# Optimization experiments

Measured on AMD Instinct MI355X. Metric: run time of the kernel, lower is better.

## Reference

```python
import jax, jax.numpy as jnp
import numpy as np

N, H, E, P = 100000, 64, 1600000, 3


def setup_inputs() -> dict:
    key = jax.random.key(0)
    ks = jax.random.split(key, 12)
    h = jax.random.normal(ks[0], (N, H), dtype=jnp.float32)
    W = jax.random.normal(ks[1], (P, H, H), dtype=jnp.float32) * 0.1
    b = jnp.zeros((P, H), dtype=jnp.float32)
    a = jnp.full((P,), 0.25, dtype=jnp.float32)  # PReLU slopes (torch default init)
    fc_w = jax.random.normal(ks[2], (H, H), dtype=jnp.float32) * 0.1
    fc_b = jnp.zeros((H,), dtype=jnp.float32)
    att = jax.random.normal(ks[3], (H,), dtype=jnp.float32) * 0.1
    adj_vals = jax.random.uniform(ks[4], (E,), dtype=jnp.float32) * (1.0 / 16.0)
    row = jax.random.randint(ks[5], (E,), 0, N, dtype=jnp.int32)
    col = jax.random.randint(ks[6], (E,), 0, N, dtype=jnp.int32)
    mask1 = jax.random.randint(ks[7], (N,), 0, 2, dtype=jnp.int32).astype(bool)
    mask2 = jax.random.randint(ks[8], (N,), 0, 2, dtype=jnp.int32).astype(bool)
    return {"h": h, "W": W, "b": b, "a": a, "fc_w": fc_w, "fc_b": fc_b,
            "att": att, "adj_vals": adj_vals, "row": row, "col": col,
            "mask1": mask1, "mask2": mask2}


def reference(h, W, b, a, fc_w, fc_b, att, adj_vals, row, col, mask1, mask2):
    n = h.shape[0]

    def gcn_all(x):
        # P GCN layers (small fixed P): linear -> spmm(adj) -> +bias -> PReLU
        outs = []
        for p in range(W.shape[0]):
            fts = x @ W[p].T                                   # [N,H]
            msg = fts[col] * adj_vals[:, None]                  # [E,H] gather
            agg = jax.ops.segment_sum(msg, row, num_segments=n) # [N,H] scatter-add
            o = agg + b[p]
            outs.append(jnp.where(o > 0, o, a[p] * o))          # PReLU
        return jnp.stack(outs)                                  # [P,N,H]

    def attention(embeds):
        # sp_p = mean_n tanh(fc(embed_p)); beta = softmax_p(att . sp_p)
        s = jnp.tanh(jnp.einsum('pnh,kh->pnk', embeds, fc_w) + fc_b).mean(axis=1)  # [P,H]
        beta = jax.nn.softmax(s @ att, axis=0)                                      # [P]
        return jnp.einsum('pnh,p->nh', embeds, beta)                                # [N,H]

    h_masked = h * (~mask1)[:, None].astype(h.dtype)
    z_mp = attention(gcn_all(h_masked))       # encode with mask_ratio1
    z_mp2 = attention(gcn_all(h))             # encode with mask_ratio 0
    z_masked = z_mp * (~mask2)[:, None].astype(h.dtype)
    x_recon = attention(gcn_all(z_masked))    # decode
    return (z_mp, z_mp2, x_recon)
```

## Files before the change

kernel.cpp:

```cpp
#include <hip/hip_runtime.h>
#include <hip/hip_bf16.h>

typedef __hip_bfloat16 bf16;
typedef __attribute__((ext_vector_type(8))) short bf16x8;
typedef __attribute__((ext_vector_type(4))) float f32x4;


__device__ __forceinline__ short f2bf(float x) {
    unsigned u = __float_as_uint(x);
    unsigned r = (u + 0x7FFFu + ((u >> 16) & 1u)) >> 16;
    return (short)r;
}
__device__ __forceinline__ float bf2f(short s) {
    return __uint_as_float(((unsigned)(unsigned short)s) << 16);
}
__device__ __forceinline__ void split1(float v, short& h, short& l) {
    h = f2bf(v);
    l = f2bf(v - bf2f(h));
}

__device__ __forceinline__ void split8(const float* __restrict__ p, bool ok, bf16x8& hi,
                                       bf16x8& lo) {
    float v[8];
    if (ok) {
        float4 x0 = ((const float4*)p)[0];
        float4 x1 = ((const float4*)p)[1];
        v[0] = x0.x; v[1] = x0.y; v[2] = x0.z; v[3] = x0.w;
        v[4] = x1.x; v[5] = x1.y; v[6] = x1.z; v[7] = x1.w;
    } else {
#pragma unroll
        for (int j = 0; j < 8; j++) v[j] = 0.f;
    }
#pragma unroll
    for (int j = 0; j < 8; j++) {
        short hb = f2bf(v[j]);
        hi[j] = hb;
        lo[j] = f2bf(v[j] - bf2f(hb));
    }
}

__device__ __forceinline__ float fast_tanh(float x) {
    x = fminf(fmaxf(x, -15.f), 15.f);
    float t = __expf(2.f * x);
    return __fdividef(t - 1.f, t + 1.f);
}

__device__ __forceinline__ void fma4(float4& acc, float v, const float4& x) {
    acc.x = fmaf(v, x.x, acc.x);
    acc.y = fmaf(v, x.y, acc.y);
    acc.z = fmaf(v, x.z, acc.z);
    acc.w = fmaf(v, x.w, acc.w);
}

__device__ __forceinline__ void red4(float4& a) {
    a.x += __shfl_xor(a.x, 16); a.y += __shfl_xor(a.y, 16);
    a.z += __shfl_xor(a.z, 16); a.w += __shfl_xor(a.w, 16);
    a.x += __shfl_xor(a.x, 32); a.y += __shfl_xor(a.y, 32);
    a.z += __shfl_xor(a.z, 32); a.w += __shfl_xor(a.w, 32);
}

__global__ __launch_bounds__(256) void forensic_kernel(const unsigned int* __restrict__ mask_w,
                                                       const unsigned int* __restrict__ idx_w,
                                                       int nw_mask, int nw_idx,
                                                       int* __restrict__ flags) {
    __shared__ int sm[6];
    int t = threadIdx.x;
    if (t < 6) sm[t] = 0;
    __syncthreads();
    int m_gt1 = 0, m_f32 = 0, m_f64 = 0, m_oddnz = 0, i_hi = 0, i_oddnz = 0;
    for (int i = t; i < nw_mask; i += 256) {
        unsigned int w = mask_w[i];
        if (w > 1u && w != 0x3F800000u && w != 0x3FF00000u) m_gt1++;
        if (w == 0x3F800000u) m_f32++;
        if ((i & 1) && w == 0x3FF00000u) m_f64++;
        if ((i & 1) && w != 0u) m_oddnz++;
    }
    for (int i = t; i < nw_idx; i += 256) {
        unsigned int v = idx_w[i];
        if (v >= 0x20000000u) i_hi++;
        if ((i & 1) && v != 0u) i_oddnz++;
    }
    atomicAdd(&sm[0], m_gt1);
    atomicAdd(&sm[1], m_f32);
    atomicAdd(&sm[2], m_f64);
    atomicAdd(&sm[3], m_oddnz);
    atomicAdd(&sm[4], i_hi);
    atomicAdd(&sm[5], i_oddnz);
    __syncthreads();
    if (t == 0) {
        int mmode;
        if (sm[1] > 50) mmode = 2;
        else if (sm[2] > 50) mmode = 4;
        else if (sm[0] > 50) mmode = 0;
        else if (sm[3] > 50) mmode = 1;
        else mmode = 3;
        int imode;
        if (sm[4] > (nw_idx * 3) / 4) imode = 2;
        else if (sm[4] > nw_idx / 4) imode = 4;
        else if (sm[5] > 50) imode = 1;
        else imode = 3;
        flags[0] = mmode;
        flags[1] = imode;
    }
}

__device__ __forceinline__ int fetch_idx(const void* p, int e, int mode) {
    switch (mode) {
        case 1: return ((const int*)p)[e];
        case 3: return (int)(((const long long*)p)[e]);
        case 2: return (int)(((const float*)p)[e]);
        default: return (int)(((const double*)p)[e]);
    }
}

__device__ __forceinline__ bool conv_one(const void* m, int mode, int i) {
    switch (mode) {
        case 0: return ((const unsigned char*)m)[i] != 0;
        case 1: return ((const int*)m)[i] != 0;
        case 2: return ((const float*)m)[i] != 0.f;
        case 3: return ((const long long*)m)[i] != 0;
        default: return ((const double*)m)[i] != 0.0;
    }
}

__global__ __launch_bounds__(256) void conv_masks(const void* __restrict__ m1,
                                                  const void* __restrict__ m2,
                                                  const int* __restrict__ flags, int n,
                                                  unsigned char* __restrict__ o1,
                                                  unsigned char* __restrict__ o2) {
    int mode = flags[0];
    int i = blockIdx.x * 256 + threadIdx.x;
    if (i >= n) return;
    o1[i] = conv_one(m1, mode, i) ? 1 : 0;
    o2[i] = conv_one(m2, mode, i) ? 1 : 0;
}


__global__ __launch_bounds__(256) void bucket_hist(const void* __restrict__ row,
                                                   const int* __restrict__ flags, int e_cnt,
                                                   int n, int shift, int nb,
                                                   int* __restrict__ bcnt) {
    __shared__ int hist[2048];
    int t = threadIdx.x;
    for (int i = t; i < nb; i += 256) hist[i] = 0;
    __syncthreads();
    int imode = flags[1];
    for (int e = blockIdx.x * 256 + t; e < e_cnt; e += gridDim.x * 256) {
        int r = fetch_idx(row, e, imode);
        if ((unsigned)r < (unsigned)n) atomicAdd(&hist[r >> shift], 1);
    }
    __syncthreads();
    for (int i = t; i < nb; i += 256)
        if (hist[i]) atomicAdd(&bcnt[i], hist[i]);
}

__global__ __launch_bounds__(1024) void bucket_scan(int* __restrict__ bptr, int nb,
                                                    int* __restrict__ bcur, int n,
                                                    int* __restrict__ row_ptr) {
    __shared__ int sh[1024];
    int t = threadIdx.x;
    int i0 = t * 2, i1 = t * 2 + 1;
    int a = (i0 < nb) ? bptr[i0] : 0;
    int b = (i1 < nb) ? bptr[i1] : 0;
    int s = a + b;
    sh[t] = s;
    __syncthreads();
    for (int off = 1; off < 1024; off <<= 1) {
        int u = (t >= off) ? sh[t - off] : 0;
        __syncthreads();
        sh[t] += u;
        __syncthreads();
    }
    int base = sh[t] - s;
    if (i0 < nb) { bptr[i0] = base; bcur[i0] = base; }
    if (i1 < nb) { bptr[i1] = base + a; bcur[i1] = base + a; }
    if (t == 1023) {
        bptr[nb] = sh[1023];
        row_ptr[n] = sh[1023];
    }
}

__global__ __launch_bounds__(256) void bin_pass2(const void* __restrict__ row,
                                                 const void* __restrict__ col,
                                                 const float* __restrict__ vals,
                                                 const int* __restrict__ flags, int e_cnt, int n,
                                                 int shift, int nb, int* __restrict__ bcur,
                                                 int2* __restrict__ rcbin,
                                                 float* __restrict__ valbin) {
    __shared__ int hist[2048];
    __shared__ int base[2048];
    int t = threadIdx.x;
    int e0 = blockIdx.x * 2048;
    if (e0 >= e_cnt) return;
    int imode = flags[1];
    for (int i = t; i < nb; i += 256) hist[i] = 0;
    __syncthreads();
    int rr[8], cc[8];
    float vv[8];
    bool ok[8];
#pragma unroll
    for (int j = 0; j < 8; j++) {
        int e = e0 + j * 256 + t;
        ok[j] = false;
        if (e < e_cnt) {
            int r = fetch_idx(row, e, imode);
            if ((unsigned)r < (unsigned)n) {
                ok[j] = true;
                rr[j] = r;
                int c = fetch_idx(col, e, imode);
                cc[j] = ((unsigned)c < (unsigned)n) ? c : 0;
                vv[j] = vals[e];
                atomicAdd(&hist[r >> shift], 1);
            }
        }
    }
    __syncthreads();
    for (int i = t; i < nb; i += 256) {
        int c = hist[i];
        base[i] = c ? atomicAdd(&bcur[i], c) : 0;
        hist[i] = 0;
    }
    __syncthreads();
#pragma unroll
    for (int j = 0; j < 8; j++) {
        if (ok[j]) {
            int bk = rr[j] >> shift;
            int pos = base[bk] + atomicAdd(&hist[bk], 1);
            rcbin[pos] = make_int2(rr[j], cc[j]);
            valbin[pos] = vv[j];
        }
    }
}

__global__ __launch_bounds__(512) void csr_finalize(const int* __restrict__ bptr,
                                                    const int2* __restrict__ rcbin,
                                                    const float* __restrict__ valbin, int n,
                                                    int shift, int* __restrict__ row_ptr,
                                                    int* __restrict__ col_s,
                                                    float* __restrict__ val_s) {
    __shared__ int cnt[1024];
    __shared__ int curs[1024];
    __shared__ int red[512];
    int b = blockIdx.x, t = threadIdx.x;
    int rpb = 1 << shift;
    int r0 = b << shift;
    int rows = n - r0;
    if (rows <= 0) return;
    if (rows > rpb) rows = rpb;
    int ebase = bptr[b], eend = bptr[b + 1];
    for (int i = t; i < rows; i += 512) cnt[i] = 0;
    __syncthreads();
    for (int e = ebase + t; e < eend; e += 512) atomicAdd(&cnt[rcbin[e].x - r0], 1);
    __syncthreads();
    int v[2], s = 0;
#pragma unroll
    for (int j = 0; j < 2; j++) {
        int idx = t * 2 + j;
        v[j] = (idx < rows) ? cnt[idx] : 0;
        s += v[j];
    }
    red[t] = s;
    __syncthreads();
    for (int off = 1; off < 512; off <<= 1) {
        int u = (t >= off) ? red[t - off] : 0;
        __syncthreads();
        red[t] += u;
        __syncthreads();
    }
    int run = ebase + red[t] - s;
#pragma unroll
    for (int j = 0; j < 2; j++) {
        int idx = t * 2 + j;
        if (idx < rows) {
            row_ptr[r0 + idx] = run;
            curs[idx] = run;
            run += v[j];
        }
    }
    __syncthreads();
    for (int e = ebase + t; e < eend; e += 512) {
        int2 rc = rcbin[e];
        float vv = valbin[e];
        int pos = atomicAdd(&curs[rc.x - r0], 1);
        col_s[pos] = rc.y;
        val_s[pos] = vv;
    }
}


__global__ __launch_bounds__(256) void spmm_dual(const float* __restrict__ X,
                                                 const int* __restrict__ row_ptr,
                                                 const int* __restrict__ col_s,
                                                 const float* __restrict__ val_s,
                                                 const unsigned char* __restrict__ mask, int n,
                                                 float* __restrict__ ax_m,
                                                 float* __restrict__ ax_f) {
    int gid = blockIdx.x * 256 + threadIdx.x;
    int r = gid >> 6;
    if (r >= n) return;
    int lane = threadIdx.x & 63;
    int g = lane >> 4, sub = lane & 15;
    int s = row_ptr[r], e = row_ptr[r + 1];
    int cnt = e - s;
    int myc = 0;
    float myvf = 0.f, myvm = 0.f;
    if (lane < cnt) {
        myc = col_s[s + lane];
        float v = val_s[s + lane];
        myvf = v;
        myvm = mask[myc] ? 0.f : v;
    }
    int cmain = cnt > 64 ? 64 : cnt;
    float4 fA = {0, 0, 0, 0}, fB = {0, 0, 0, 0}, mA = {0, 0, 0, 0}, mB = {0, 0, 0, 0};
    for (int i = 0; i < cmain; i += 16) {
        int i0 = i + g, i1 = i + 4 + g, i2 = i + 8 + g, i3 = i + 12 + g;
        int c0 = __shfl(myc, i0), c1 = __shfl(myc, i1);
        int c2 = __shfl(myc, i2), c3 = __shfl(myc, i3);
        float vf0 = __shfl(myvf, i0), vf1 = __shfl(myvf, i1);
        float vf2 = __shfl(myvf, i2), vf3 = __shfl(myvf, i3);
        float vm0 = __shfl(myvm, i0), vm1 = __shfl(myvm, i1);
        float vm2 = __shfl(myvm, i2), vm3 = __shfl(myvm, i3);
        if (i0 < cmain) {
            float4 x = *(const float4*)(X + (size_t)c0 * 64 + sub * 4);
            fma4(fA, vf0, x);
            fma4(mA, vm0, x);
        }
        if (i1 < cmain) {
            float4 x = *(const float4*)(X + (size_t)c1 * 64 + sub * 4);
            fma4(fB, vf1, x);
            fma4(mB, vm1, x);
        }
        if (i2 < cmain) {
            float4 x = *(const float4*)(X + (size_t)c2 * 64 + sub * 4);
            fma4(fA, vf2, x);
            fma4(mA, vm2, x);
        }
        if (i3 < cmain) {
            float4 x = *(const float4*)(X + (size_t)c3 * 64 + sub * 4);
            fma4(fB, vf3, x);
            fma4(mB, vm3, x);
        }
    }
    for (int i = 64 + g; i < cnt; i += 4) {
        int c = col_s[s + i];
        float v = val_s[s + i];
        float vm = mask[c] ? 0.f : v;
        float4 x = *(const float4*)(X + (size_t)c * 64 + sub * 4);
        fma4(fA, v, x);
        fma4(mA, vm, x);
    }
    fA.x += fB.x; fA.y += fB.y; fA.z += fB.z; fA.w += fB.w;
    mA.x += mB.x; mA.y += mB.y; mA.z += mB.z; mA.w += mB.w;
    red4(fA);
    red4(mA);
    if (g == 0) {
        *(float4*)(ax_f + (size_t)r * 64 + sub * 4) = fA;
        *(float4*)(ax_m + (size_t)r * 64 + sub * 4) = mA;
    }
}

__global__ __launch_bounds__(256) void spmm_one(const float* __restrict__ X,
                                                const int* __restrict__ row_ptr,
                                                const int* __restrict__ col_s,
                                                const float* __restrict__ val_s,
                                                const unsigned char* __restrict__ mask, int n,
                                                float* __restrict__ ax) {
    int gid = blockIdx.x * 256 + threadIdx.x;
    int r = gid >> 6;
    if (r >= n) return;
    int lane = threadIdx.x & 63;
    int g = lane >> 4, sub = lane & 15;
    int s = row_ptr[r], e = row_ptr[r + 1];
    int cnt = e - s;
    int myc = 0;
    float myv = 0.f;
    if (lane < cnt) {
        myc = col_s[s + lane];
        float v = val_s[s + lane];
        myv = mask[myc] ? 0.f : v;
    }
    int cmain = cnt > 64 ? 64 : cnt;
    float4 aA = {0, 0, 0, 0}, aB = {0, 0, 0, 0};
    for (int i = 0; i < cmain; i += 16) {
        int i0 = i + g, i1 = i + 4 + g, i2 = i + 8 + g, i3 = i + 12 + g;
        int c0 = __shfl(myc, i0), c1 = __shfl(myc, i1);
        int c2 = __shfl(myc, i2), c3 = __shfl(myc, i3);
        float v0 = __shfl(myv, i0), v1 = __shfl(myv, i1);
        float v2 = __shfl(myv, i2), v3 = __shfl(myv, i3);
        if (i0 < cmain && v0 != 0.f) {
            float4 x = *(const float4*)(X + (size_t)c0 * 64 + sub * 4);
            fma4(aA, v0, x);
        }
        if (i1 < cmain && v1 != 0.f) {
            float4 x = *(const float4*)(X + (size_t)c1 * 64 + sub * 4);
            fma4(aB, v1, x);
        }
        if (i2 < cmain && v2 != 0.f) {
            float4 x = *(const float4*)(X + (size_t)c2 * 64 + sub * 4);
            fma4(aA, v2, x);
        }
        if (i3 < cmain && v3 != 0.f) {
            float4 x = *(const float4*)(X + (size_t)c3 * 64 + sub * 4);
            fma4(aB, v3, x);
        }
    }
    for (int i = 64 + g; i < cnt; i += 4) {
        int c = col_s[s + i];
        if (mask[c]) continue;
        float v = val_s[s + i];
        float4 x = *(const float4*)(X + (size_t)c * 64 + sub * 4);
        fma4(aA, v, x);
    }
    aA.x += aB.x; aA.y += aB.y; aA.z += aB.z; aA.w += aB.w;
    red4(aA);
    if (g == 0) *(float4*)(ax + (size_t)r * 64 + sub * 4) = aA;
}


template <int PP>
__global__ __launch_bounds__(256) void gemm_tanh(const float* __restrict__ X,
                                                 const float* __restrict__ Wg,
                                                 const float* __restrict__ b,
                                                 const float* __restrict__ a,
                                                 const float* __restrict__ fcw,
                                                 const float* __restrict__ fcb, int n,
                                                 float* __restrict__ s_sums) {
    __shared__ __align__(16) short xhi[16][72], xlo[16][72];
    __shared__ __align__(16) short ehi[PP][16][72], elo[PP][16][72];
    int t = threadIdx.x;
    int wv = t >> 6, lane = t & 63, nl = lane & 15, q = lane >> 4;
    int colg = wv * 16 + nl;
    int srow = t >> 4, scol = (t & 15) * 4;
    bf16x8 whi[PP][2], wlo[PP][2];
    float bias[PP], slope[PP];
#pragma unroll
    for (int p = 0; p < PP; p++) {
#pragma unroll
        for (int kk = 0; kk < 2; kk++)
            split8(Wg + p * 4096 + colg * 64 + kk * 32 + q * 8, true, whi[p][kk], wlo[p][kk]);
        bias[p] = b[p * 64 + colg];
        slope[p] = a[p];
    }
    bf16x8 fhi[2], flo[2];
#pragma unroll
    for (int kk = 0; kk < 2; kk++)
        split8(fcw + colg * 64 + kk * 32 + q * 8, true, fhi[kk], flo[kk]);
    float fbias = fcb[colg];
    float ssum[PP];
#pragma unroll
    for (int p = 0; p < PP; p++) ssum[p] = 0.f;

    int ntiles = (n + 15) >> 4;
    for (int rt = blockIdx.x; rt < ntiles; rt += gridDim.x) {
        int gr = rt * 16 + srow;
        float4 xv = (gr < n) ? *(const float4*)(X + (size_t)gr * 64 + scol)
                             : make_float4(0.f, 0.f, 0.f, 0.f);
        short4 hh, ll;
        split1(xv.x, hh.x, ll.x);
        split1(xv.y, hh.y, ll.y);
        split1(xv.z, hh.z, ll.z);
        split1(xv.w, hh.w, ll.w);
        *(short4*)(&xhi[srow][scol]) = hh;
        *(short4*)(&xlo[srow][scol]) = ll;
        __syncthreads();
        bf16x8 ah[2], al[2];
#pragma unroll
        for (int kk = 0; kk < 2; kk++) {
            ah[kk] = *(const bf16x8*)(&xhi[nl][kk * 32 + q * 8]);
            al[kk] = *(const bf16x8*)(&xlo[nl][kk * 32 + q * 8]);
        }
#pragma unroll
        for (int p = 0; p < PP; p++) {
            f32x4 acc = {0.f, 0.f, 0.f, 0.f};
            acc = __builtin_amdgcn_mfma_f32_16x16x32_bf16(ah[0], whi[p][0], acc, 0, 0, 0);
            acc = __builtin_amdgcn_mfma_f32_16x16x32_bf16(ah[1], whi[p][1], acc, 0, 0, 0);
            acc = __builtin_amdgcn_mfma_f32_16x16x32_bf16(al[0], whi[p][0], acc, 0, 0, 0);
            acc = __builtin_amdgcn_mfma_f32_16x16x32_bf16(al[1], whi[p][1], acc, 0, 0, 0);
            acc = __builtin_amdgcn_mfma_f32_16x16x32_bf16(ah[0], wlo[p][0], acc, 0, 0, 0);
            acc = __builtin_amdgcn_mfma_f32_16x16x32_bf16(ah[1], wlo[p][1], acc, 0, 0, 0);
            acc = __builtin_amdgcn_mfma_f32_16x16x32_bf16(al[0], wlo[p][0], acc, 0, 0, 0);
            acc = __builtin_amdgcn_mfma_f32_16x16x32_bf16(al[1], wlo[p][1], acc, 0, 0, 0);
#pragma unroll
            for (int i = 0; i < 4; i++) {
                float o = acc[i] + bias[p];
                o = (o > 0.f) ? o : slope[p] * o;
                short hb, lb;
                split1(o, hb, lb);
                ehi[p][q * 4 + i][colg] = hb;
                elo[p][q * 4 + i][colg] = lb;
            }
        }
        __syncthreads();
#pragma unroll
        for (int p = 0; p < PP; p++) {
            bf16x8 eh[2], el[2];
#pragma unroll
            for (int kk = 0; kk < 2; kk++) {
                eh[kk] = *(const bf16x8*)(&ehi[p][nl][kk * 32 + q * 8]);
                el[kk] = *(const bf16x8*)(&elo[p][nl][kk * 32 + q * 8]);
            }
            f32x4 acc = {0.f, 0.f, 0.f, 0.f};
            acc = __builtin_amdgcn_mfma_f32_16x16x32_bf16(eh[0], fhi[0], acc, 0, 0, 0);
            acc = __builtin_amdgcn_mfma_f32_16x16x32_bf16(eh[1], fhi[1], acc, 0, 0, 0);
            acc = __builtin_amdgcn_mfma_f32_16x16x32_bf16(el[0], fhi[0], acc, 0, 0, 0);
            acc = __builtin_amdgcn_mfma_f32_16x16x32_bf16(el[1], fhi[1], acc, 0, 0, 0);
            acc = __builtin_amdgcn_mfma_f32_16x16x32_bf16(eh[0], flo[0], acc, 0, 0, 0);
            acc = __builtin_amdgcn_mfma_f32_16x16x32_bf16(eh[1], flo[1], acc, 0, 0, 0);
#pragma unroll
            for (int i = 0; i < 4; i++) {
                int r = rt * 16 + q * 4 + i;
                if (r < n) ssum[p] += fast_tanh(acc[i] + fbias);
            }
        }
    }
#pragma unroll
    for (int p = 0; p < PP; p++) {
        float s = ssum[p];
        s += __shfl_xor(s, 16);
        s += __shfl_xor(s, 32);
        if (q == 0) atomicAdd(&s_sums[p * 64 + colg], s);
    }
}


template <int PP>
__global__ __launch_bounds__(256) void gemm_mix(const float* __restrict__ X,
                                                const float* __restrict__ Wg,
                                                const float* __restrict__ b,
                                                const float* __restrict__ a,
                                                const float* __restrict__ beta, int n,
                                                float* __restrict__ out, int accum) {
    int t = threadIdx.x;
    int wv = t >> 6, lane = t & 63, nl = lane & 15, q = lane >> 4;
    int colg = wv * 16 + nl;
    bf16x8 whi[PP][2], wlo[PP][2];
    float bias[PP], slope[PP], bet[PP];
#pragma unroll
    for (int p = 0; p < PP; p++) {
#pragma unroll
        for (int kk = 0; kk < 2; kk++)
            split8(Wg + p * 4096 + colg * 64 + kk * 32 + q * 8, true, whi[p][kk], wlo[p][kk]);
        bias[p] = b[p * 64 + colg];
        slope[p] = a[p];
        bet[p] = beta[p];
    }
    int ntiles = (n + 15) >> 4;
    for (int rt = blockIdx.x; rt < ntiles; rt += gridDim.x) {
        int rowi = rt * 16 + nl;
        bool ok = rowi < n;
        bf16x8 ah[2], al[2];
#pragma unroll
        for (int kk = 0; kk < 2; kk++)
            split8(X + (size_t)rowi * 64 + kk * 32 + q * 8, ok, ah[kk], al[kk]);
        float mix[4] = {0.f, 0.f, 0.f, 0.f};
#pragma unroll
        for (int p = 0; p < PP; p++) {
            f32x4 acc = {0.f, 0.f, 0.f, 0.f};
            acc = __builtin_amdgcn_mfma_f32_16x16x32_bf16(ah[0], whi[p][0], acc, 0, 0, 0);
            acc = __builtin_amdgcn_mfma_f32_16x16x32_bf16(ah[1], whi[p][1], acc, 0, 0, 0);
            acc = __builtin_amdgcn_mfma_f32_16x16x32_bf16(al[0], whi[p][0], acc, 0, 0, 0);
            acc = __builtin_amdgcn_mfma_f32_16x16x32_bf16(al[1], whi[p][1], acc, 0, 0, 0);
            acc = __builtin_amdgcn_mfma_f32_16x16x32_bf16(ah[0], wlo[p][0], acc, 0, 0, 0);
            acc = __builtin_amdgcn_mfma_f32_16x16x32_bf16(ah[1], wlo[p][1], acc, 0, 0, 0);
            acc = __builtin_amdgcn_mfma_f32_16x16x32_bf16(al[0], wlo[p][0], acc, 0, 0, 0);
            acc = __builtin_amdgcn_mfma_f32_16x16x32_bf16(al[1], wlo[p][1], acc, 0, 0, 0);
#pragma unroll
            for (int i = 0; i < 4; i++) {
                float o = acc[i] + bias[p];
                o = (o > 0.f) ? o : slope[p] * o;
                mix[i] = fmaf(bet[p], o, mix[i]);
            }
        }
#pragma unroll
        for (int i = 0; i < 4; i++) {
            int r = rt * 16 + q * 4 + i;
            if (r < n) {
                size_t idx = (size_t)r * 64 + colg;
                out[idx] = accum ? (out[idx] + mix[i]) : mix[i];
            }
        }
    }
}

__global__ __launch_bounds__(64) void compute_beta(const float* __restrict__ s_sums,
                                                   const float* __restrict__ att, int n, int P,
                                                   float* __restrict__ beta) {
    int lane = threadIdx.x;
    float av = att[lane];
    float l[8];
    for (int p = 0; p < P; p++) l[p] = s_sums[p * 64 + lane] * av;
#pragma unroll
    for (int off = 32; off > 0; off >>= 1)
        for (int p = 0; p < 8; p++)
            if (p < P) l[p] += __shfl_down(l[p], off);
    if (lane == 0) {
        const float inv = 1.0f / (float)n;
        float m = -1e30f;
        for (int p = 0; p < P; p++) {
            l[p] *= inv;
            m = fmaxf(m, l[p]);
        }
        float s = 0.f;
        for (int p = 0; p < P; p++) {
            l[p] = __expf(l[p] - m);
            s += l[p];
        }
        for (int p = 0; p < P; p++) beta[p] = l[p] / s;
    }
}


extern "C" void kernel_launch(void* const* d_in, const int* in_sizes, int n_in,
                              void* d_out, int out_size, void* d_ws, size_t ws_size,
                              hipStream_t stream) {
    const float* h = (const float*)d_in[0];
    const float* W = (const float*)d_in[1];
    const float* b = (const float*)d_in[2];
    const float* a = (const float*)d_in[3];
    const float* fc_w = (const float*)d_in[4];
    const float* fc_b = (const float*)d_in[5];
    const float* att = (const float*)d_in[6];
    const float* adj = (const float*)d_in[7];
    const void* row = d_in[8];
    const void* col = d_in[9];
    const void* mask1 = d_in[10];
    const void* mask2 = d_in[11];
    float* out = (float*)d_out;

    int P = in_sizes[3];
    if (P < 1 || P > 8) P = 3;
    int N = in_sizes[0] / 64;
    int E = in_sizes[7];

    int shift = 8;
    while (((N >> shift) + 1) > 2048) shift++;
    int NB = (N >> shift) + 1;

    char* w = (char*)d_ws;
    auto alloc = [&](size_t bytes) {
        void* p = (void*)w;
        w += (bytes + 255) & ~(size_t)255;
        return p;
    };
    int* row_ptr = (int*)alloc((size_t)(N + 1) * 4);
    int* col_s = (int*)alloc((size_t)E * 4);
    float* val_s = (float*)alloc((size_t)E * 4);
    int* bptr = (int*)alloc((size_t)(NB + 1) * 4);
    int* bcur = (int*)alloc((size_t)NB * 4);
    int2* rcbin = (int2*)alloc((size_t)E * 8);
    float* valbin = (float*)alloc((size_t)E * 4);
    unsigned char* m1c = (unsigned char*)alloc(N);
    unsigned char* m2c = (unsigned char*)alloc(N);
    float* axm = (float*)alloc((size_t)N * 64 * 4);
    float* axf = (float*)alloc((size_t)N * 64 * 4);
    float* s_sums = (float*)alloc(8 * 64 * 4);
    float* beta = (float*)alloc(8 * 4);
    int* flags = (int*)alloc(256);

    int nw_mask = N / 4 > 25000 ? 25000 : N / 4;
    int nw_idx = E / 4 > 25000 ? 25000 : E / 4;
    forensic_kernel<<<1, 256, 0, stream>>>((const unsigned int*)mask1, (const unsigned int*)row,
                                           nw_mask, nw_idx, flags);
    conv_masks<<<(N + 255) / 256, 256, 0, stream>>>(mask1, mask2, flags, N, m1c, m2c);

    hipMemsetAsync(bptr, 0, (size_t)(NB + 1) * 4, stream);
    bucket_hist<<<1024, 256, 0, stream>>>(row, flags, E, N, shift, NB, bptr);
    bucket_scan<<<1, 1024, 0, stream>>>(bptr, NB, bcur, N, row_ptr);
    int bin_blocks = (E + 2047) / 2048;
    bin_pass2<<<bin_blocks, 256, 0, stream>>>(row, col, adj, flags, E, N, shift, NB, bcur, rcbin,
                                              valbin);
    csr_finalize<<<NB, 512, 0, stream>>>(bptr, rcbin, valbin, N, shift, row_ptr, col_s, val_s);

    int spmm_grid = ((size_t)N * 64 + 255) / 256;
    int tanh_blocks = 2048;
    int mix_blocks = 1536;

    auto tail = [&](const float* ax, float* dst) {
        hipMemsetAsync(s_sums, 0, 8 * 64 * 4, stream);
        if (P == 3) {
            gemm_tanh<3><<<tanh_blocks, 256, 0, stream>>>(ax, W, b, a, fc_w, fc_b, N, s_sums);
        } else {
            for (int p = 0; p < P; p++)
                gemm_tanh<1><<<tanh_blocks, 256, 0, stream>>>(ax, W + p * 4096, b + p * 64, a + p,
                                                              fc_w, fc_b, N, s_sums + p * 64);
        }
        compute_beta<<<1, 64, 0, stream>>>(s_sums, att, N, P, beta);
        if (P == 3) {
            gemm_mix<3><<<mix_blocks, 256, 0, stream>>>(ax, W, b, a, beta, N, dst, 0);
        } else {
            for (int p = 0; p < P; p++)
                gemm_mix<1><<<mix_blocks, 256, 0, stream>>>(ax, W + p * 4096, b + p * 64, a + p,
                                                            beta + p, N, dst, p != 0);
        }
    };

    spmm_dual<<<spmm_grid, 256, 0, stream>>>(h, row_ptr, col_s, val_s, m1c, N, axm, axf);
    tail(axm, out);
    tail(axf, out + (size_t)N * 64);
    spmm_one<<<spmm_grid, 256, 0, stream>>>(out, row_ptr, col_s, val_s, m2c, N, axm);
    tail(axm, out + (size_t)2 * N * 64);
}
```

Before: 664.9 us.

## Store SpMM outputs pre-split as bf16 hi/lo and prefetch GEMM tiles

The SpMM kernels now write their aggregated rows directly as split bf16 hi/lo planes instead of fp32. The tanh and mix GEMM kernels load these planes straight into MFMA operand registers, dropping the shared-memory staging and the repeated split work. Each kernel also prefetches the next row tile into registers while computing the current one. Buffers are padded to a multiple of 16 rows with memsets, and grid sizes are changed to 1024 blocks. The written bytes stay the same (two shorts per float), and the extra registers used for prefetch may reduce occupancy.

```diff
diff --git a/kernel.cpp b/kernel.cpp
--- a/kernel.cpp
+++ b/kernel.cpp
@@ -293,8 +293,10 @@
                                                  const int* __restrict__ col_s,
                                                  const float* __restrict__ val_s,
                                                  const unsigned char* __restrict__ mask, int n,
-                                                 float* __restrict__ ax_m,
-                                                 float* __restrict__ ax_f) {
+                                                 short* __restrict__ axm_hi,
+                                                 short* __restrict__ axm_lo,
+                                                 short* __restrict__ axf_hi,
+                                                 short* __restrict__ axf_lo) {
     int gid = blockIdx.x * 256 + threadIdx.x;
     int r = gid >> 6;
     if (r >= n) return;
@@ -354,8 +356,16 @@
     red4(fA);
     red4(mA);
     if (g == 0) {
-        *(float4*)(ax_f + (size_t)r * 64 + sub * 4) = fA;
-        *(float4*)(ax_m + (size_t)r * 64 + sub * 4) = mA;
+        size_t o = (size_t)r * 64 + sub * 4;
+        short4 h4, l4;
+        split1(fA.x, h4.x, l4.x); split1(fA.y, h4.y, l4.y);
+        split1(fA.z, h4.z, l4.z); split1(fA.w, h4.w, l4.w);
+        *(short4*)(axf_hi + o) = h4;
+        *(short4*)(axf_lo + o) = l4;
+        split1(mA.x, h4.x, l4.x); split1(mA.y, h4.y, l4.y);
+        split1(mA.z, h4.z, l4.z); split1(mA.w, h4.w, l4.w);
+        *(short4*)(axm_hi + o) = h4;
+        *(short4*)(axm_lo + o) = l4;
     }
 }
 
@@ -364,7 +374,8 @@
                                                 const int* __restrict__ col_s,
                                                 const float* __restrict__ val_s,
                                                 const unsigned char* __restrict__ mask, int n,
-                                                float* __restrict__ ax) {
+                                                short* __restrict__ ax_hi,
+                                                short* __restrict__ ax_lo) {
     int gid = blockIdx.x * 256 + threadIdx.x;
     int r = gid >> 6;
     if (r >= n) return;
@@ -413,24 +424,30 @@
     }
     aA.x += aB.x; aA.y += aB.y; aA.z += aB.z; aA.w += aB.w;
     red4(aA);
-    if (g == 0) *(float4*)(ax + (size_t)r * 64 + sub * 4) = aA;
+    if (g == 0) {
+        size_t o = (size_t)r * 64 + sub * 4;
+        short4 h4, l4;
+        split1(aA.x, h4.x, l4.x); split1(aA.y, h4.y, l4.y);
+        split1(aA.z, h4.z, l4.z); split1(aA.w, h4.w, l4.w);
+        *(short4*)(ax_hi + o) = h4;
+        *(short4*)(ax_lo + o) = l4;
+    }
 }
 
 
 template <int PP>
-__global__ __launch_bounds__(256) void gemm_tanh(const float* __restrict__ X,
+__global__ __launch_bounds__(256) void gemm_tanh(const short* __restrict__ Xhi,
+                                                 const short* __restrict__ Xlo,
                                                  const float* __restrict__ Wg,
                                                  const float* __restrict__ b,
                                                  const float* __restrict__ a,
                                                  const float* __restrict__ fcw,
-                                                 const float* __restrict__ fcb, int n,
+                                                 const float* __restrict__ fcb, int n, int ntiles,
                                                  float* __restrict__ s_sums) {
-    __shared__ __align__(16) short xhi[16][72], xlo[16][72];
     __shared__ __align__(16) short ehi[PP][16][72], elo[PP][16][72];
     int t = threadIdx.x;
     int wv = t >> 6, lane = t & 63, nl = lane & 15, q = lane >> 4;
     int colg = wv * 16 + nl;
-    int srow = t >> 4, scol = (t & 15) * 4;
     bf16x8 whi[PP][2], wlo[PP][2];
     float bias[PP], slope[PP];
 #pragma unroll
@@ -450,25 +467,17 @@
 #pragma unroll
     for (int p = 0; p < PP; p++) ssum[p] = 0.f;
 
-    int ntiles = (n + 15) >> 4;
-    for (int rt = blockIdx.x; rt < ntiles; rt += gridDim.x) {
-        int gr = rt * 16 + srow;
-        float4 xv = (gr < n) ? *(const float4*)(X + (size_t)gr * 64 + scol)
-                             : make_float4(0.f, 0.f, 0.f, 0.f);
-        short4 hh, ll;
-        split1(xv.x, hh.x, ll.x);
-        split1(xv.y, hh.y, ll.y);
-        split1(xv.z, hh.z, ll.z);
-        split1(xv.w, hh.w, ll.w);
-        *(short4*)(&xhi[srow][scol]) = hh;
-        *(short4*)(&xlo[srow][scol]) = ll;
-        __syncthreads();
-        bf16x8 ah[2], al[2];
+    int rt = blockIdx.x;
+    bf16x8 ah[2], al[2];
+    if (rt < ntiles) {
+        size_t rb = (size_t)(rt * 16 + nl) * 64 + q * 8;
 #pragma unroll
         for (int kk = 0; kk < 2; kk++) {
-            ah[kk] = *(const bf16x8*)(&xhi[nl][kk * 32 + q * 8]);
-            al[kk] = *(const bf16x8*)(&xlo[nl][kk * 32 + q * 8]);
-        }
+            ah[kk] = *(const bf16x8*)(Xhi + rb + kk * 32);
+            al[kk] = *(const bf16x8*)(Xlo + rb + kk * 32);
+        }
+    }
+    for (; rt < ntiles; rt += gridDim.x) {
 #pragma unroll
         for (int p = 0; p < PP; p++) {
             f32x4 acc = {0.f, 0.f, 0.f, 0.f};
@@ -488,6 +497,16 @@
                 split1(o, hb, lb);
                 ehi[p][q * 4 + i][colg] = hb;
                 elo[p][q * 4 + i][colg] = lb;
+            }
+        }
+        int rn = rt + gridDim.x;
+        bf16x8 pfh[2], pfl[2];
+        if (rn < ntiles) {
+            size_t rb = (size_t)(rn * 16 + nl) * 64 + q * 8;
+#pragma unroll
+            for (int kk = 0; kk < 2; kk++) {
+                pfh[kk] = *(const bf16x8*)(Xhi + rb + kk * 32);
+                pfl[kk] = *(const bf16x8*)(Xlo + rb + kk * 32);
             }
         }
         __syncthreads();
@@ -512,6 +531,12 @@
                 if (r < n) ssum[p] += fast_tanh(acc[i] + fbias);
             }
         }
+        __syncthreads();
+#pragma unroll
+        for (int kk = 0; kk < 2; kk++) {
+            ah[kk] = pfh[kk];
+            al[kk] = pfl[kk];
+        }
     }
 #pragma unroll
     for (int p = 0; p < PP; p++) {
@@ -524,11 +549,12 @@
 
 
 template <int PP>
-__global__ __launch_bounds__(256) void gemm_mix(const float* __restrict__ X,
+__global__ __launch_bounds__(256) void gemm_mix(const short* __restrict__ Xhi,
+                                                const short* __restrict__ Xlo,
                                                 const float* __restrict__ Wg,
                                                 const float* __restrict__ b,
                                                 const float* __restrict__ a,
-                                                const float* __restrict__ beta, int n,
+                                                const float* __restrict__ beta, int n, int ntiles,
                                                 float* __restrict__ out, int accum) {
     int t = threadIdx.x;
     int wv = t >> 6, lane = t & 63, nl = lane & 15, q = lane >> 4;
@@ -544,14 +570,27 @@
         slope[p] = a[p];
         bet[p] = beta[p];
     }
-    int ntiles = (n + 15) >> 4;
-    for (int rt = blockIdx.x; rt < ntiles; rt += gridDim.x) {
-        int rowi = rt * 16 + nl;
-        bool ok = rowi < n;
-        bf16x8 ah[2], al[2];
-#pragma unroll
-        for (int kk = 0; kk < 2; kk++)
-            split8(X + (size_t)rowi * 64 + kk * 32 + q * 8, ok, ah[kk], al[kk]);
+    int rt = blockIdx.x;
+    bf16x8 ah[2], al[2];
+    if (rt < ntiles) {
+        size_t rb = (size_t)(rt * 16 + nl) * 64 + q * 8;
+#pragma unroll
+        for (int kk = 0; kk < 2; kk++) {
+            ah[kk] = *(const bf16x8*)(Xhi + rb + kk * 32);
+            al[kk] = *(const bf16x8*)(Xlo + rb + kk * 32);
+        }
+    }
+    for (; rt < ntiles; rt += gridDim.x) {
+        int rn = rt + gridDim.x;
+        bf16x8 pfh[2], pfl[2];
+        if (rn < ntiles) {
+            size_t rb = (size_t)(rn * 16 + nl) * 64 + q * 8;
+#pragma unroll
+            for (int kk = 0; kk < 2; kk++) {
+                pfh[kk] = *(const bf16x8*)(Xhi + rb + kk * 32);
+                pfl[kk] = *(const bf16x8*)(Xlo + rb + kk * 32);
+            }
+        }
         float mix[4] = {0.f, 0.f, 0.f, 0.f};
 #pragma unroll
         for (int p = 0; p < PP; p++) {
@@ -578,6 +617,11 @@
                 size_t idx = (size_t)r * 64 + colg;
                 out[idx] = accum ? (out[idx] + mix[i]) : mix[i];
             }
+        }
+#pragma unroll
+        for (int kk = 0; kk < 2; kk++) {
+            ah[kk] = pfh[kk];
+            al[kk] = pfl[kk];
         }
     }
 }
@@ -631,6 +675,8 @@
     if (P < 1 || P > 8) P = 3;
     int N = in_sizes[0] / 64;
     int E = in_sizes[7];
+    int N16 = (N + 15) & ~15;
+    int ntiles = N16 >> 4;
 
     int shift = 8;
     while (((N >> shift) + 1) > 2048) shift++;
@@ -651,8 +697,10 @@
     float* valbin = (float*)alloc((size_t)E * 4);
     unsigned char* m1c = (unsigned char*)alloc(N);
     unsigned char* m2c = (unsigned char*)alloc(N);
-    float* axm = (float*)alloc((size_t)N * 64 * 4);
-    float* axf = (float*)alloc((size_t)N * 64 * 4);
+    short* axm_hi = (short*)alloc((size_t)N16 * 64 * 2);
+    short* axm_lo = (short*)alloc((size_t)N16 * 64 * 2);
+    short* axf_hi = (short*)alloc((size_t)N16 * 64 * 2);
+    short* axf_lo = (short*)alloc((size_t)N16 * 64 * 2);
     float* s_sums = (float*)alloc(8 * 64 * 4);
     float* beta = (float*)alloc(8 * 4);
     int* flags = (int*)alloc(256);
@@ -664,6 +712,13 @@
     conv_masks<<<(N + 255) / 256, 256, 0, stream>>>(mask1, mask2, flags, N, m1c, m2c);
 
     hipMemsetAsync(bptr, 0, (size_t)(NB + 1) * 4, stream);
+    if (N16 > N) {
+        size_t padoff = (size_t)N * 64, padbytes = (size_t)(N16 - N) * 64 * 2;
+        hipMemsetAsync(axm_hi + padoff, 0, padbytes, stream);
+        hipMemsetAsync(axm_lo + padoff, 0, padbytes, stream);
+        hipMemsetAsync(axf_hi + padoff, 0, padbytes, stream);
+        hipMemsetAsync(axf_lo + padoff, 0, padbytes, stream);
+    }
     bucket_hist<<<1024, 256, 0, stream>>>(row, flags, E, N, shift, NB, bptr);
     bucket_scan<<<1, 1024, 0, stream>>>(bptr, NB, bcur, N, row_ptr);
     int bin_blocks = (E + 2047) / 2048;
@@ -672,31 +727,36 @@
     csr_finalize<<<NB, 512, 0, stream>>>(bptr, rcbin, valbin, N, shift, row_ptr, col_s, val_s);
 
     int spmm_grid = ((size_t)N * 64 + 255) / 256;
-    int tanh_blocks = 2048;
-    int mix_blocks = 1536;
-
-    auto tail = [&](const float* ax, float* dst) {
+    int tanh_blocks = 1024;
+    int mix_blocks = 1024;
+
+    auto tail = [&](const short* axhi, const short* axlo, float* dst) {
         hipMemsetAsync(s_sums, 0, 8 * 64 * 4, stream);
         if (P == 3) {
-            gemm_tanh<3><<<tanh_blocks, 256, 0, stream>>>(ax, W, b, a, fc_w, fc_b, N, s_sums);
+            gemm_tanh<3><<<tanh_blocks, 256, 0, stream>>>(axhi, axlo, W, b, a, fc_w, fc_b, N,
+                                                          ntiles, s_sums);
         } else {
             for (int p = 0; p < P; p++)
-                gemm_tanh<1><<<tanh_blocks, 256, 0, stream>>>(ax, W + p * 4096, b + p * 64, a + p,
-                                                              fc_w, fc_b, N, s_sums + p * 64);
+                gemm_tanh<1><<<tanh_blocks, 256, 0, stream>>>(axhi, axlo, W + p * 4096,
+                                                              b + p * 64, a + p, fc_w, fc_b, N,
+                                                              ntiles, s_sums + p * 64);
         }
         compute_beta<<<1, 64, 0, stream>>>(s_sums, att, N, P, beta);
         if (P == 3) {
-            gemm_mix<3><<<mix_blocks, 256, 0, stream>>>(ax, W, b, a, beta, N, dst, 0);
+            gemm_mix<3><<<mix_blocks, 256, 0, stream>>>(axhi, axlo, W, b, a, beta, N, ntiles, dst,
+                                                        0);
         } else {
             for (int p = 0; p < P; p++)
-                gemm_mix<1><<<mix_blocks, 256, 0, stream>>>(ax, W + p * 4096, b + p * 64, a + p,
-                                                            beta + p, N, dst, p != 0);
+                gemm_mix<1><<<mix_blocks, 256, 0, stream>>>(axhi, axlo, W + p * 4096, b + p * 64,
+                                                            a + p, beta + p, N, ntiles, dst,
+                                                            p != 0);
         }
     };
 
-    spmm_dual<<<spmm_grid, 256, 0, stream>>>(h, row_ptr, col_s, val_s, m1c, N, axm, axf);
-    tail(axm, out);
-    tail(axf, out + (size_t)N * 64);
-    spmm_one<<<spmm_grid, 256, 0, stream>>>(out, row_ptr, col_s, val_s, m2c, N, axm);
-    tail(axm, out + (size_t)2 * N * 64);
-}
+    spmm_dual<<<spmm_grid, 256, 0, stream>>>(h, row_ptr, col_s, val_s, m1c, N, axm_hi, axm_lo,
+                                             axf_hi, axf_lo);
+    tail(axm_hi, axm_lo, out);
+    tail(axf_hi, axf_lo, out + (size_t)N * 64);
+    spmm_one<<<spmm_grid, 256, 0, stream>>>(out, row_ptr, col_s, val_s, m2c, N, axm_hi, axm_lo);
+    tail(axm_hi, axm_lo, out + (size_t)2 * N * 64);
+}
```

Result: faster. 591.2 us (-11.1%).
